# Kernel optimization log

Hardware: AMD Instinct MI355X
Metric: run time of the kernel (lower is better)

The kernel has to match this reference:

```python
import jax, jax.numpy as jnp
import numpy as np
import math

B, H, W = 4, 256, 256
S = 256          # num_superpixels
ZD = 128         # z_dim
GC = 256         # g_channels
NBLK = 8


def setup_inputs() -> dict:
    key = jax.random.key(0)
    ks = jax.random.split(key, 12)
    rn = lambda k, shp, s=1.0: jax.random.normal(k, shp, jnp.float32) * s
    return {
        "z": rn(ks[0], (B, ZD)),
        "images": rn(ks[1], (B, 3, H, W)),
        "segments": jax.random.randint(ks[2], (B, H, W), 0, S).astype(jnp.int32),
        # row-stochastic-ish adjacency scale keeps 8 propagations stable
        "A": rn(ks[3], (B, S, S), 1.0 / math.sqrt(S)),
        # WSConv2d weights: init N(0,1); forward multiplies input by sqrt(2/(in*k*k))
        "proj_w": rn(ks[4], (GC, 3 + ZD)), "proj_b": jnp.zeros((GC,), jnp.float32),
        "blk_proj_w": rn(ks[5], (NBLK, GC, GC)), "blk_proj_b": jnp.zeros((NBLK, GC), jnp.float32),
        "ada1_w": rn(ks[6], (NBLK, 2 * GC, GC)), "ada1_b": jnp.zeros((NBLK, 2 * GC), jnp.float32),
        "ada2_w": rn(ks[7], (NBLK, 2 * GC, 2 * GC)), "ada2_b": jnp.zeros((NBLK, 2 * GC), jnp.float32),
        # plain Conv2d 3x3 layers in upsample head
        "up1_w": rn(ks[8], (GC // 2, GC, 3, 3), 0.02), "up1_b": jnp.zeros((GC // 2,), jnp.float32),
        "up2_w": rn(ks[9], (3, GC // 2, 3, 3), 0.02), "up2_b": jnp.zeros((3,), jnp.float32),
    }


def _ws1x1(x, w, b):
    # WSConv2d with 1x1 kernel over node dim: x [B,Cin,S] -> [B,Cout,S]
    scale = math.sqrt(2.0 / w.shape[1])
    return jnp.einsum('oc,bcs->bos', w, x) * scale + b[None, :, None]


def _conv3(x, w, b):
    y = jax.lax.conv_general_dilated(x, w, (1, 1), 'SAME',
                                     dimension_numbers=('NCHW', 'OIHW', 'NCHW'))
    return y + b[None, :, None, None]


def _forward(z, images, A, proj_w, proj_b, blk_proj_w, blk_proj_b,
             ada1_w, ada1_b, ada2_w, ada2_b, up1_w, up1_b, up2_w, up2_b,
             segments):
    Bn, _, Hn, Wn = images.shape
    N = Hn * Wn
    flat = images.reshape(Bn, 3, N)            # [B,3,N]
    seg = segments.reshape(Bn, N)              # [B,N] int

    # superpixel mean pooling (math of one_hot^T @ flat / counts, as segment-sum)
    seg_sum = jax.vmap(lambda f, s: jax.ops.segment_sum(f, s, num_segments=S))(
        flat.transpose(0, 2, 1), seg)          # [B,S,3]
    counts = jax.vmap(lambda s: jax.ops.segment_sum(
        jnp.ones(s.shape, jnp.float32), s, num_segments=S))(seg)  # [B,S]
    feats = seg_sum / (counts[..., None] + 1e-6)

    z_rep = jnp.broadcast_to(z[:, None, :], (Bn, S, ZD))
    x = jnp.concatenate([feats, z_rep], axis=2).transpose(0, 2, 1)  # [B,3+ZD,S]
    x = _ws1x1(x, proj_w, proj_b)                                   # [B,GC,S]

    for i in range(NBLK):
        h = _ws1x1(x, blk_proj_w[i], blk_proj_b[i])
        # A @ feat : out[b,c,i] = sum_j A[b,i,j] h[b,c,j]
        h = jnp.einsum('bij,bcj->bci', A, h)
        # AdaIN: style from global mean over nodes
        m = h.mean(axis=2, keepdims=True)                    # [B,GC,1]
        s1 = jax.nn.leaky_relu(_ws1x1(m, ada1_w[i], ada1_b[i]), 0.2)
        style = _ws1x1(s1, ada2_w[i], ada2_b[i])             # [B,2GC,1]
        gamma, beta = jnp.split(style, 2, axis=1)
        h = gamma * h + beta
        x = jax.nn.leaky_relu(h, 0.2)                        # dropout=0 (eval)

    # broadcast superpixel feats back to pixels (math of one_hot @ sup_feats)
    sup_feats = x.transpose(0, 2, 1)                         # [B,S,GC]
    pix = jnp.take_along_axis(sup_feats, seg[:, :, None].astype(jnp.int32), axis=1)  # [B,N,GC]
    pix = pix.transpose(0, 2, 1).reshape(Bn, GC, Hn, Wn)

    y = jax.nn.leaky_relu(_conv3(pix, up1_w, up1_b), 0.2)
    y = _conv3(y, up2_w, up2_b)                              # [B,3,H,W]
    # InstanceNorm2d(3), affine=False, eps=1e-5
    mu = y.mean((2, 3), keepdims=True)
    var = y.var((2, 3), keepdims=True)
    y = (y - mu) / jnp.sqrt(var + 1e-5)
    return jnp.tanh(y)


def reference(z, images, segments, A, proj_w, proj_b, blk_proj_w, blk_proj_b,
              ada1_w, ada1_b, ada2_w, ada2_b, up1_w, up1_b, up2_w, up2_b):
    return _forward(z, images, A, proj_w, proj_b, blk_proj_w, blk_proj_b,
                    ada1_w, ada1_b, ada2_w, ada2_b, up1_w, up1_b, up2_w, up2_b,
                    segments)
```

## Files before the change

### kernel.cpp

```cpp
#include <hip/hip_runtime.h>
#include <cmath>

#define BB 4
#define SS 256
#define ZDIM 128
#define GCH 256
#define NBLKS 8
#define NPIX 65536
#define U1C 128

__device__ __forceinline__ float lrelu(float x){ return x >= 0.f ? x : 0.2f*x; }

__global__ void k_pool(const float* __restrict__ img, const int* __restrict__ seg,
                       float* __restrict__ segsum, float* __restrict__ counts){
  __shared__ float ls[SS*4];
  int t = threadIdx.x;
  for(int j=t;j<SS*4;j+=256) ls[j]=0.f;
  __syncthreads();
  int b = blockIdx.x >> 6;
  int base = blockIdx.x*1024;
  for(int it=0; it<4; it++){
    int idx = base + it*256 + t;
    int n = idx & (NPIX-1);
    int s = seg[idx];
    atomicAdd(&ls[s*4+0], img[(b*3+0)*NPIX+n]);
    atomicAdd(&ls[s*4+1], img[(b*3+1)*NPIX+n]);
    atomicAdd(&ls[s*4+2], img[(b*3+2)*NPIX+n]);
    atomicAdd(&ls[s*4+3], 1.0f);
  }
  __syncthreads();
  for(int j=t;j<SS*4;j+=256){
    int s = j>>2, c = j&3;
    float vv = ls[j];
    if(vv != 0.f){
      if(c<3) atomicAdd(&segsum[(b*SS+s)*3+c], vv);
      else    atomicAdd(&counts[b*SS+s], vv);
    }
  }
}

__global__ __launch_bounds__(256) void k_prepA(const float* __restrict__ A,
                                               float* __restrict__ At){
  __shared__ float t[32][33];
  int b = blockIdx.z;
  int bx = blockIdx.x*32, by = blockIdx.y*32;
  int lx = threadIdx.x & 31, ly4 = (threadIdx.x >> 5)*4;
  #pragma unroll
  for(int r=0;r<4;r++)
    t[ly4+r][lx] = A[(b<<16) + ((by+ly4+r)<<8) + bx + lx];
  __syncthreads();
  #pragma unroll
  for(int r=0;r<4;r++)
    At[(b<<16) + ((bx+ly4+r)<<8) + by + lx] = t[lx][ly4+r];
}

__global__ void k_prepW(const float* __restrict__ w1, const float* __restrict__ w2,
                        float* __restrict__ wT, float* __restrict__ w2t){
  int idx = blockIdx.x*256 + threadIdx.x;
  if(idx < 294912){
    int o = idx & 127; int r = idx >> 7; int c = r & 255; int k = r >> 8;
    wT[idx] = w1[(o*GCH + c)*9 + k];
  } else if(idx < 294912 + 3456){
    int t = idx - 294912;
    int cc = t & 7;
    int oc = (t >> 3) % 3;
    int sg = (t / 24) & 3;
    int g  = (t / 96) & 3;
    int k  = t / 384;
    w2t[t] = w2[oc*1152 + (g*32 + sg*8 + cc)*9 + k];
  }
}

__global__ void k_x0(const float* __restrict__ segsum, const float* __restrict__ counts,
                     const float* __restrict__ z, const float* __restrict__ pw,
                     const float* __restrict__ pb, float sc, float* __restrict__ xp){
  int i = blockIdx.x*64 + (threadIdx.x & 63);
  int o = blockIdx.y*4  + (threadIdx.x >> 6);
  int b = blockIdx.z;
  float cnt = counts[b*SS+i] + 1e-6f;
  float f0 = segsum[(b*SS+i)*3+0]/cnt;
  float f1 = segsum[(b*SS+i)*3+1]/cnt;
  float f2 = segsum[(b*SS+i)*3+2]/cnt;
  const float* wr = pw + o*131;
  float acc = wr[0]*f0 + wr[1]*f1 + wr[2]*f2;
  const float* zb = z + b*ZDIM;
  #pragma unroll 8
  for(int j=0;j<ZDIM;j++) acc += wr[3+j]*zb[j];
  xp[(b*GCH+o)*SS + i] = acc*sc + pb[o];
}

__global__ __launch_bounds__(512) void k_gemm(const float* __restrict__ xp,
        const float* __restrict__ bw, const float* __restrict__ bb,
        const float* __restrict__ At, float sc,
        float* __restrict__ h2, float* __restrict__ m){
  int c0 = blockIdx.x*4;
  int b  = blockIdx.y;
  int j  = threadIdx.x & 255;
  int half = threadIdx.x >> 8;
  __shared__ float wl[4][256];
  __shared__ float h1l[4][260];
  __shared__ float red[4][4];
  wl[half*2+0][j] = bw[(c0+half*2+0)*GCH + j];
  wl[half*2+1][j] = bw[(c0+half*2+1)*GCH + j];
  __syncthreads();
  const float* xb = xp + b*GCH*SS + j;
  float a0 = 0.f, a1 = 0.f;
  int ch = half*2;
  #pragma unroll 8
  for(int k=0;k<GCH;k++){
    float xv = xb[k*SS];
    a0 += wl[ch][k]*xv;
    a1 += wl[ch+1][k]*xv;
  }
  h1l[ch][j]   = a0*sc + bb[c0+ch];
  h1l[ch+1][j] = a1*sc + bb[c0+ch+1];
  __syncthreads();
  const float* ab = At + b*SS*SS + j;
  float r0 = 0.f, r1 = 0.f;
  #pragma unroll 2
  for(int jj=0;jj<SS;jj+=4){
    float4 h0 = *(const float4*)&h1l[ch][jj];
    float4 h1v = *(const float4*)&h1l[ch+1][jj];
    float av0 = ab[jj*SS], av1 = ab[(jj+1)*SS], av2 = ab[(jj+2)*SS], av3 = ab[(jj+3)*SS];
    r0 += h0.x*av0 + h0.y*av1 + h0.z*av2 + h0.w*av3;
    r1 += h1v.x*av0 + h1v.y*av1 + h1v.z*av2 + h1v.w*av3;
  }
  h2[(b*GCH+c0+ch)*SS + j]   = r0;
  h2[(b*GCH+c0+ch+1)*SS + j] = r1;
  float s0 = r0, s1v = r1;
  for(int off=32; off; off>>=1){ s0 += __shfl_down(s0,off); s1v += __shfl_down(s1v,off); }
  int w3 = (threadIdx.x >> 6) & 3;
  if((j&63)==0){ red[ch][w3] = s0; red[ch+1][w3] = s1v; }
  __syncthreads();
  if(threadIdx.x < 4)
    m[b*GCH + c0 + threadIdx.x] =
      (red[threadIdx.x][0]+red[threadIdx.x][1]+red[threadIdx.x][2]+red[threadIdx.x][3])*(1.f/256.f);
}

__global__ __launch_bounds__(512) void k_s12(const float* __restrict__ m,
        const float* __restrict__ a1w, const float* __restrict__ a1b,
        const float* __restrict__ a2w, const float* __restrict__ a2b,
        const float* __restrict__ h2, float sc1, float sc2, float* __restrict__ xp){
  int q = blockIdx.x;
  int tid = threadIdx.x;
  int lane = tid & 63, wv = tid >> 6;
  int grp = lane >> 3, ll = lane & 7;
  __shared__ float4 ml4[256];
  __shared__ float s1l[4][512];
  __shared__ float gbl[4][16];
  if(tid < 256) ml4[tid] = ((const float4*)m)[tid];
  __syncthreads();
  #pragma unroll 2
  for(int pass=0; pass<8; pass++){
    int row = wv*64 + pass*8 + grp;
    const float4* ar = (const float4*)(a1w + row*GCH) + ll;
    float p0=0.f,p1=0.f,p2=0.f,p3=0.f;
    #pragma unroll
    for(int j=0;j<8;j++){
      float4 w4 = ar[j*8];
      float4 m0 = ml4[0*64 + j*8 + ll];
      float4 m1 = ml4[1*64 + j*8 + ll];
      float4 m2 = ml4[2*64 + j*8 + ll];
      float4 m3 = ml4[3*64 + j*8 + ll];
      p0 += w4.x*m0.x + w4.y*m0.y + w4.z*m0.z + w4.w*m0.w;
      p1 += w4.x*m1.x + w4.y*m1.y + w4.z*m1.z + w4.w*m1.w;
      p2 += w4.x*m2.x + w4.y*m2.y + w4.z*m2.z + w4.w*m2.w;
      p3 += w4.x*m3.x + w4.y*m3.y + w4.z*m3.z + w4.w*m3.w;
    }
    #pragma unroll
    for(int off=1; off<8; off<<=1){
      p0 += __shfl_xor(p0,off); p1 += __shfl_xor(p1,off);
      p2 += __shfl_xor(p2,off); p3 += __shfl_xor(p3,off);
    }
    if(ll == 0){
      float bv = a1b[row];
      int sidx = ((row & 7) << 6) + (row >> 3);
      s1l[0][sidx] = lrelu(p0*sc1 + bv);
      s1l[1][sidx] = lrelu(p1*sc1 + bv);
      s1l[2][sidx] = lrelu(p2*sc1 + bv);
      s1l[3][sidx] = lrelu(p3*sc1 + bv);
    }
  }
  __syncthreads();
  float sA[4][8];
  #pragma unroll
  for(int b=0;b<4;b++)
    #pragma unroll
    for(int j=0;j<8;j++) sA[b][j] = s1l[b][j*64 + lane];
  #pragma unroll
  for(int r=0;r<2;r++){
    int ridx = wv*2 + r;
    int cc = ridx & 7;
    int t = (ridx < 8) ? (q*8 + cc) : (256 + q*8 + cc);
    const float* wr = a2w + t*512 + lane*8;
    float4 wa = *(const float4*)wr;
    float4 wb4 = *(const float4*)(wr+4);
    float p0 = wa.x*sA[0][0]+wa.y*sA[0][1]+wa.z*sA[0][2]+wa.w*sA[0][3]
             + wb4.x*sA[0][4]+wb4.y*sA[0][5]+wb4.z*sA[0][6]+wb4.w*sA[0][7];
    float p1 = wa.x*sA[1][0]+wa.y*sA[1][1]+wa.z*sA[1][2]+wa.w*sA[1][3]
             + wb4.x*sA[1][4]+wb4.y*sA[1][5]+wb4.z*sA[1][6]+wb4.w*sA[1][7];
    float p2 = wa.x*sA[2][0]+wa.y*sA[2][1]+wa.z*sA[2][2]+wa.w*sA[2][3]
             + wb4.x*sA[2][4]+wb4.y*sA[2][5]+wb4.z*sA[2][6]+wb4.w*sA[2][7];
    float p3 = wa.x*sA[3][0]+wa.y*sA[3][1]+wa.z*sA[3][2]+wa.w*sA[3][3]
             + wb4.x*sA[3][4]+wb4.y*sA[3][5]+wb4.z*sA[3][6]+wb4.w*sA[3][7];
    for(int off=32; off; off>>=1){
      p0 += __shfl_xor(p0,off); p1 += __shfl_xor(p1,off);
      p2 += __shfl_xor(p2,off); p3 += __shfl_xor(p3,off);
    }
    if(lane < 4){
      float p = lane==0 ? p0 : lane==1 ? p1 : lane==2 ? p2 : p3;
      gbl[lane][ridx] = p*sc2 + a2b[t];
    }
  }
  __syncthreads();
  int c0 = q*8;
  int jn = tid & 255;
  int hf = tid >> 8;
  #pragma unroll
  for(int b=0;b<4;b++){
    #pragma unroll
    for(int c2=0;c2<4;c2++){
      int cc = hf*4 + c2;
      float ga = gbl[b][cc], be = gbl[b][8+cc];
      float hv = h2[(b*GCH + c0+cc)*SS + jn];
      xp[(b*GCH + c0+cc)*SS + jn] = lrelu(ga*hv + be);
    }
  }
}

__global__ __launch_bounds__(256) void k_v(const float* __restrict__ xf,
        const float4* __restrict__ wT4, float4* __restrict__ v4){
  int s0 = blockIdx.x*16;
  int k  = blockIdx.y;
  int b  = blockIdx.z;
  int tid = threadIdx.x;
  __shared__ float4 wl[64][33];
  __shared__ float xft[256][16];
  for(int t = tid; t < 1024; t += 256){
    int c = t>>2, sf = t&3;
    *(float4*)&xft[c][sf*4] = *(const float4*)(xf + (b*GCH+c)*SS + s0 + sf*4);
  }
  int og = tid & 31, sh = tid >> 5;
  const float4* wb = wT4 + (size_t)k*GCH*32;
  float4 a0 = {0.f,0.f,0.f,0.f}, a1 = {0.f,0.f,0.f,0.f};
  for(int ct=0; ct<4; ct++){
    __syncthreads();
    for(int t = tid; t < 2048; t += 256){
      int cc = t>>5, o = t&31;
      wl[cc][o] = wb[(ct*64+cc)*32 + o];
    }
    __syncthreads();
    #pragma unroll 4
    for(int cc=0;cc<64;cc++){
      float4 w = wl[cc][og];
      int c = ct*64+cc;
      float x0v = xft[c][sh];
      float x1v = xft[c][8+sh];
      a0.x += w.x*x0v; a0.y += w.y*x0v; a0.z += w.z*x0v; a0.w += w.w*x0v;
      a1.x += w.x*x1v; a1.y += w.y*x1v; a1.z += w.z*x1v; a1.w += w.w*x1v;
    }
  }
  size_t base = (size_t)(b*9+k)*SS + s0;
  v4[(base + sh)*32 + og]     = a0;
  v4[(base + 8 + sh)*32 + og] = a1;
}

__global__ __launch_bounds__(256) void k_conv(const float4* __restrict__ v4,
        const int* __restrict__ seg, const float4* __restrict__ b14,
        const float* __restrict__ w2t, float* __restrict__ y2){
  __shared__ float4 y1t4[100*9];
  __shared__ int   segl[144];
  __shared__ float part[768];
  int bid = blockIdx.x;
  int x = bid & 7;
  int b = x >> 1;
  int sub = ((bid >> 3) << 1) + (x & 1);
  int g = sub & 3;
  int tile = sub >> 2;
  int x0p = (tile & 31)*8, y0p = (tile >> 5)*8;
  int tid = threadIdx.x;
  if(tid < 144){
    int r = tid/12, cc = tid%12;
    int gy = y0p - 2 + r, gx = x0p - 2 + cc;
    segl[tid] = (gy>=0 && gy<256 && gx>=0 && gx<256) ? seg[(b*256+gy)*256+gx] : -1;
  }
  __syncthreads();
  int o4 = tid & 7;
  const float4* vb = v4 + (size_t)(b*9)*SS*32 + g*8 + o4;
  float4 bias = b14[g*8 + o4];
  bool interior = (x0p >= 8 && x0p <= 240 && y0p >= 8 && y0p <= 240);
  if(interior){
    for(int task = tid; task < 800; task += 256){
      int pp = task >> 3;
      int py = pp/10, px = pp - py*10;
      float4 acc = bias;
      #pragma unroll
      for(int k=0;k<9;k++){
        int sidx = segl[(py + k/3)*12 + (px + k%3)];
        float4 vv = vb[(k*SS + sidx)*32];
        acc.x += vv.x; acc.y += vv.y; acc.z += vv.z; acc.w += vv.w;
      }
      float4 val;
      val.x = lrelu(acc.x); val.y = lrelu(acc.y);
      val.z = lrelu(acc.z); val.w = lrelu(acc.w);
      y1t4[pp*9 + o4] = val;
    }
  } else {
    for(int task = tid; task < 800; task += 256){
      int pp = task >> 3;
      int py = pp/10, px = pp - py*10;
      int gy = y0p - 1 + py, gx = x0p - 1 + px;
      bool pix_ok = (gy>=0 && gy<256 && gx>=0 && gx<256);
      float4 acc = bias;
      #pragma unroll
      for(int k=0;k<9;k++){
        int sidx = segl[(py + k/3)*12 + (px + k%3)];
        int sidx0 = sidx < 0 ? 0 : sidx;
        float msk = sidx < 0 ? 0.f : 1.f;
        float4 vv = vb[(k*SS + sidx0)*32];
        acc.x += msk*vv.x; acc.y += msk*vv.y; acc.z += msk*vv.z; acc.w += msk*vv.w;
      }
      float4 val;
      val.x = pix_ok ? lrelu(acc.x) : 0.f;
      val.y = pix_ok ? lrelu(acc.y) : 0.f;
      val.z = pix_ok ? lrelu(acc.z) : 0.f;
      val.w = pix_ok ? lrelu(acc.w) : 0.f;
      y1t4[pp*9 + o4] = val;
    }
  }
  __syncthreads();
  int pxo = tid & 63, sg = tid >> 6;
  int sgu = __builtin_amdgcn_readfirstlane(sg);
  const float* wk0 = w2t + (g*4 + sgu)*24;
  int ty = pxo >> 3, tx = pxo & 7;
  float p0=0.f,p1=0.f,p2=0.f;
  #pragma unroll
  for(int k=0;k<9;k++){
    int pp0 = (ty + k/3)*10 + (tx + k%3);
    float4 ya = y1t4[pp0*9 + sgu*2];
    float4 yb = y1t4[pp0*9 + sgu*2 + 1];
    const float* wk = wk0 + k*384;
    p0 += wk[0]*ya.x + wk[1]*ya.y + wk[2]*ya.z + wk[3]*ya.w
        + wk[4]*yb.x + wk[5]*yb.y + wk[6]*yb.z + wk[7]*yb.w;
    p1 += wk[8]*ya.x + wk[9]*ya.y + wk[10]*ya.z + wk[11]*ya.w
        + wk[12]*yb.x + wk[13]*yb.y + wk[14]*yb.z + wk[15]*yb.w;
    p2 += wk[16]*ya.x + wk[17]*ya.y + wk[18]*ya.z + wk[19]*ya.w
        + wk[20]*yb.x + wk[21]*yb.y + wk[22]*yb.z + wk[23]*yb.w;
  }
  part[tid]     = p0;
  part[256+tid] = p1;
  part[512+tid] = p2;
  __syncthreads();
  if(tid < 64){
    float s0 = part[tid]    +part[tid+64]    +part[tid+128]    +part[tid+192];
    float s1 = part[256+tid]+part[256+tid+64]+part[256+tid+128]+part[256+tid+192];
    float s2 = part[512+tid]+part[512+tid+64]+part[512+tid+128]+part[512+tid+192];
    int gy = y0p + (tid>>3), gx = x0p + (tid&7);
    int nidx = gy*256+gx;
    atomicAdd(&y2[(b*3+0)*NPIX+nidx], s0);
    atomicAdd(&y2[(b*3+1)*NPIX+nidx], s1);
    atomicAdd(&y2[(b*3+2)*NPIX+nidx], s2);
  }
}

__global__ void k_stats(const float* __restrict__ y2, double* __restrict__ stats){
  int bc = blockIdx.x;
  int chunk = blockIdx.y;
  const float* p = y2 + (size_t)bc*NPIX + chunk*8192;
  int t = threadIdx.x;
  double s=0.0, q=0.0;
  for(int i=t;i<8192;i+=256){ double vv = (double)p[i]; s+=vv; q+=vv*vv; }
  __shared__ double rs[256], rq[256];
  rs[t]=s; rq[t]=q; __syncthreads();
  for(int st=128; st; st>>=1){ if(t<st){rs[t]+=rs[t+st]; rq[t]+=rq[t+st];} __syncthreads(); }
  if(t==0){ atomicAdd(&stats[bc*2], rs[0]); atomicAdd(&stats[bc*2+1], rq[0]); }
}

__global__ void k_norm(const float* __restrict__ y2, const double* __restrict__ stats,
                       float* __restrict__ out){
  int idx = blockIdx.x*256+threadIdx.x;
  int bu = idx >> 16;
  double mu  = stats[bu*2+0] * (1.0/65536.0);
  double ex2 = stats[bu*2+1] * (1.0/65536.0);
  double var = ex2 - mu*mu;
  float inv = (float)(1.0/sqrt(var + 1e-5));
  float mf = (float)mu;
  out[idx] = tanhf((y2[idx]-mf)*inv);
}

extern "C" void kernel_launch(void* const* d_in, const int* in_sizes, int n_in,
                              void* d_out, int out_size, void* d_ws, size_t ws_size,
                              hipStream_t stream) {
  const float* z   = (const float*)d_in[0];
  const float* img = (const float*)d_in[1];
  const int*   seg = (const int*)d_in[2];
  const float* A   = (const float*)d_in[3];
  const float* pw  = (const float*)d_in[4];
  const float* pb  = (const float*)d_in[5];
  const float* bw  = (const float*)d_in[6];
  const float* bb  = (const float*)d_in[7];
  const float* a1w = (const float*)d_in[8];
  const float* a1b = (const float*)d_in[9];
  const float* a2w = (const float*)d_in[10];
  const float* a2b = (const float*)d_in[11];
  const float* w1  = (const float*)d_in[12];
  const float* b1  = (const float*)d_in[13];
  const float* w2  = (const float*)d_in[14];
  const float* b2  = (const float*)d_in[15]; (void)b2;
  float* out = (float*)d_out;

  float* ws = (float*)d_ws;
  float* segsum = ws;
  float* counts = ws + 3072;
  float* m      = ws + 4096;
  double* stats = (double*)(ws + 5120);
  float* xp  = ws + 5248;
  float* h2  = xp + 262144;
  float* At  = h2 + 262144;
  float* wT  = At + 262144;
  float* v   = wT + 294912;
  float* y2  = v + 1179648;
  float* w2t = y2 + 786432;

  hipMemsetAsync(ws, 0, 5248*sizeof(float), stream);
  hipMemsetAsync(y2, 0, 786432*sizeof(float), stream);

  float sProj = (float)sqrt(2.0/131.0);
  float s256  = (float)sqrt(2.0/256.0);
  float s512  = (float)sqrt(2.0/512.0);

  k_pool <<<256, 256, 0, stream>>>(img, seg, segsum, counts);
  k_prepA<<<dim3(8,8,4), 256, 0, stream>>>(A, At);
  k_prepW<<<1166, 256, 0, stream>>>(w1, w2, wT, w2t);
  k_x0   <<<dim3(4,64,4), 256, 0, stream>>>(segsum, counts, z, pw, pb, sProj, xp);

  for(int blk=0; blk<NBLKS; blk++){
    k_gemm<<<dim3(64,4), 512, 0, stream>>>(xp, bw + blk*GCH*GCH, bb + blk*GCH,
                                           At, s256, h2, m);
    k_s12 <<<32, 512, 0, stream>>>(m, a1w + blk*512*GCH, a1b + blk*512,
                                   a2w + blk*512*512, a2b + blk*512,
                                   h2, s256, s512, xp);
  }

  k_v   <<<dim3(16,9,4), 256, 0, stream>>>(xp, (const float4*)wT, (float4*)v);
  k_conv<<<16384, 256, 0, stream>>>((const float4*)v, seg, (const float4*)b1, w2t, y2);
  k_stats<<<dim3(12,8), 256, 0, stream>>>(y2, stats);
  k_norm<<<3072, 256, 0, stream>>>(y2, stats, out);
}
```

Before: 408.7 us.

## Fuse pooling, projection and graph blocks into persistent kernel with grid barriers

```diff
diff --git a/kernel.cpp b/kernel.cpp
--- a/kernel.cpp
+++ b/kernel.cpp
@@ -11,220 +11,203 @@
 
 __device__ __forceinline__ float lrelu(float x){ return x >= 0.f ? x : 0.2f*x; }
 
-__global__ void k_pool(const float* __restrict__ img, const int* __restrict__ seg,
-                       float* __restrict__ segsum, float* __restrict__ counts){
-  __shared__ float ls[SS*4];
-  int t = threadIdx.x;
-  for(int j=t;j<SS*4;j+=256) ls[j]=0.f;
+__device__ __forceinline__ void gridbar(int* bar, int target){
   __syncthreads();
-  int b = blockIdx.x >> 6;
-  int base = blockIdx.x*1024;
-  for(int it=0; it<4; it++){
-    int idx = base + it*256 + t;
-    int n = idx & (NPIX-1);
-    int s = seg[idx];
-    atomicAdd(&ls[s*4+0], img[(b*3+0)*NPIX+n]);
-    atomicAdd(&ls[s*4+1], img[(b*3+1)*NPIX+n]);
-    atomicAdd(&ls[s*4+2], img[(b*3+2)*NPIX+n]);
-    atomicAdd(&ls[s*4+3], 1.0f);
+  if(threadIdx.x == 0){
+    __hip_atomic_fetch_add(bar, 1, __ATOMIC_RELEASE, __HIP_MEMORY_SCOPE_AGENT);
+    while(__hip_atomic_load(bar, __ATOMIC_ACQUIRE, __HIP_MEMORY_SCOPE_AGENT) < target)
+      __builtin_amdgcn_s_sleep(2);
   }
   __syncthreads();
-  for(int j=t;j<SS*4;j+=256){
-    int s = j>>2, c = j&3;
-    float vv = ls[j];
-    if(vv != 0.f){
-      if(c<3) atomicAdd(&segsum[(b*SS+s)*3+c], vv);
-      else    atomicAdd(&counts[b*SS+s], vv);
-    }
-  }
-}
-
-__global__ __launch_bounds__(256) void k_prepA(const float* __restrict__ A,
-                                               float* __restrict__ At){
-  __shared__ float t[32][33];
-  int b = blockIdx.z;
-  int bx = blockIdx.x*32, by = blockIdx.y*32;
-  int lx = threadIdx.x & 31, ly4 = (threadIdx.x >> 5)*4;
-  #pragma unroll
-  for(int r=0;r<4;r++)
-    t[ly4+r][lx] = A[(b<<16) + ((by+ly4+r)<<8) + bx + lx];
-  __syncthreads();
-  #pragma unroll
-  for(int r=0;r<4;r++)
-    At[(b<<16) + ((bx+ly4+r)<<8) + by + lx] = t[lx][ly4+r];
-}
-
-__global__ void k_prepW(const float* __restrict__ w1, const float* __restrict__ w2,
-                        float* __restrict__ wT, float* __restrict__ w2t){
-  int idx = blockIdx.x*256 + threadIdx.x;
-  if(idx < 294912){
-    int o = idx & 127; int r = idx >> 7; int c = r & 255; int k = r >> 8;
-    wT[idx] = w1[(o*GCH + c)*9 + k];
-  } else if(idx < 294912 + 3456){
-    int t = idx - 294912;
-    int cc = t & 7;
-    int oc = (t >> 3) % 3;
-    int sg = (t / 24) & 3;
-    int g  = (t / 96) & 3;
-    int k  = t / 384;
-    w2t[t] = w2[oc*1152 + (g*32 + sg*8 + cc)*9 + k];
-  }
-}
-
-__global__ void k_x0(const float* __restrict__ segsum, const float* __restrict__ counts,
-                     const float* __restrict__ z, const float* __restrict__ pw,
-                     const float* __restrict__ pb, float sc, float* __restrict__ xp){
-  int i = blockIdx.x*64 + (threadIdx.x & 63);
-  int o = blockIdx.y*4  + (threadIdx.x >> 6);
-  int b = blockIdx.z;
-  float cnt = counts[b*SS+i] + 1e-6f;
-  float f0 = segsum[(b*SS+i)*3+0]/cnt;
-  float f1 = segsum[(b*SS+i)*3+1]/cnt;
-  float f2 = segsum[(b*SS+i)*3+2]/cnt;
-  const float* wr = pw + o*131;
-  float acc = wr[0]*f0 + wr[1]*f1 + wr[2]*f2;
-  const float* zb = z + b*ZDIM;
-  #pragma unroll 8
-  for(int j=0;j<ZDIM;j++) acc += wr[3+j]*zb[j];
-  xp[(b*GCH+o)*SS + i] = acc*sc + pb[o];
-}
-
-__global__ __launch_bounds__(512) void k_gemm(const float* __restrict__ xp,
-        const float* __restrict__ bw, const float* __restrict__ bb,
-        const float* __restrict__ At, float sc,
-        float* __restrict__ h2, float* __restrict__ m){
-  int c0 = blockIdx.x*4;
-  int b  = blockIdx.y;
-  int j  = threadIdx.x & 255;
-  int half = threadIdx.x >> 8;
+}
+
+__global__ __launch_bounds__(256) void k_prep(const float* __restrict__ A,
+        const float* __restrict__ w1, const float* __restrict__ w2,
+        float* __restrict__ At, float* __restrict__ wT, float* __restrict__ w2t){
+  int bid = blockIdx.x;
+  if(bid < 256){
+    __shared__ float t[32][33];
+    int b = bid >> 6;
+    int bx = (bid & 7)*32, by = ((bid >> 3) & 7)*32;
+    int lx = threadIdx.x & 31, ly4 = (threadIdx.x >> 5)*4;
+    #pragma unroll
+    for(int r=0;r<4;r++)
+      t[ly4+r][lx] = A[(b<<16) + ((by+ly4+r)<<8) + bx + lx];
+    __syncthreads();
+    #pragma unroll
+    for(int r=0;r<4;r++)
+      At[(b<<16) + ((bx+ly4+r)<<8) + by + lx] = t[lx][ly4+r];
+  } else {
+    int idx = (bid-256)*256 + threadIdx.x;
+    if(idx < 294912){
+      int o = idx & 127; int r = idx >> 7; int c = r & 255; int k = r >> 8;
+      wT[idx] = w1[(o*GCH + c)*9 + k];
+    } else if(idx < 294912 + 3456){
+      int t2 = idx - 294912;
+      int cc = t2 & 7;
+      int oc = (t2 >> 3) % 3;
+      int sg = (t2 / 24) & 3;
+      int g  = (t2 / 96) & 3;
+      int k  = t2 / 384;
+      w2t[t2] = w2[oc*1152 + (g*32 + sg*8 + cc)*9 + k];
+    }
+  }
+}
+
+__global__ __launch_bounds__(512) void k_mega(
+    const float* __restrict__ img, const int* __restrict__ seg,
+    float* __restrict__ segsum, float* __restrict__ counts,
+    const float* __restrict__ z, const float* __restrict__ pw,
+    const float* __restrict__ pb, const float* __restrict__ At,
+    const float* __restrict__ bw_all, const float* __restrict__ bb_all,
+    const float* __restrict__ a1w_all, const float* __restrict__ a1b_all,
+    const float* __restrict__ a2w_all, const float* __restrict__ a2b_all,
+    float* __restrict__ xp, float* __restrict__ h2,
+    float* __restrict__ m, float* __restrict__ s1g, int* __restrict__ bar,
+    float sProj, float sc1, float sc2){
+  int bid = blockIdx.x;
+  int tid = threadIdx.x;
+  int lane = tid & 63, wv = tid >> 6;
+  __shared__ float ls[1024];
   __shared__ float wl[4][256];
   __shared__ float h1l[4][260];
   __shared__ float red[4][4];
-  wl[half*2+0][j] = bw[(c0+half*2+0)*GCH + j];
-  wl[half*2+1][j] = bw[(c0+half*2+1)*GCH + j];
-  __syncthreads();
-  const float* xb = xp + b*GCH*SS + j;
-  float a0 = 0.f, a1 = 0.f;
-  int ch = half*2;
-  #pragma unroll 8
-  for(int k=0;k<GCH;k++){
-    float xv = xb[k*SS];
-    a0 += wl[ch][k]*xv;
-    a1 += wl[ch+1][k]*xv;
-  }
-  h1l[ch][j]   = a0*sc + bb[c0+ch];
-  h1l[ch+1][j] = a1*sc + bb[c0+ch+1];
-  __syncthreads();
-  const float* ab = At + b*SS*SS + j;
-  float r0 = 0.f, r1 = 0.f;
-  #pragma unroll 2
-  for(int jj=0;jj<SS;jj+=4){
-    float4 h0 = *(const float4*)&h1l[ch][jj];
-    float4 h1v = *(const float4*)&h1l[ch+1][jj];
-    float av0 = ab[jj*SS], av1 = ab[(jj+1)*SS], av2 = ab[(jj+2)*SS], av3 = ab[(jj+3)*SS];
-    r0 += h0.x*av0 + h0.y*av1 + h0.z*av2 + h0.w*av3;
-    r1 += h1v.x*av0 + h1v.y*av1 + h1v.z*av2 + h1v.w*av3;
-  }
-  h2[(b*GCH+c0+ch)*SS + j]   = r0;
-  h2[(b*GCH+c0+ch+1)*SS + j] = r1;
-  float s0 = r0, s1v = r1;
-  for(int off=32; off; off>>=1){ s0 += __shfl_down(s0,off); s1v += __shfl_down(s1v,off); }
-  int w3 = (threadIdx.x >> 6) & 3;
-  if((j&63)==0){ red[ch][w3] = s0; red[ch+1][w3] = s1v; }
-  __syncthreads();
-  if(threadIdx.x < 4)
-    m[b*GCH + c0 + threadIdx.x] =
-      (red[threadIdx.x][0]+red[threadIdx.x][1]+red[threadIdx.x][2]+red[threadIdx.x][3])*(1.f/256.f);
-}
-
-__global__ __launch_bounds__(512) void k_s12(const float* __restrict__ m,
-        const float* __restrict__ a1w, const float* __restrict__ a1b,
-        const float* __restrict__ a2w, const float* __restrict__ a2b,
-        const float* __restrict__ h2, float sc1, float sc2, float* __restrict__ xp){
-  int q = blockIdx.x;
-  int tid = threadIdx.x;
-  int lane = tid & 63, wv = tid >> 6;
-  int grp = lane >> 3, ll = lane & 7;
-  __shared__ float4 ml4[256];
-  __shared__ float s1l[4][512];
-  __shared__ float gbl[4][16];
-  if(tid < 256) ml4[tid] = ((const float4*)m)[tid];
-  __syncthreads();
-  #pragma unroll 2
-  for(int pass=0; pass<8; pass++){
-    int row = wv*64 + pass*8 + grp;
-    const float4* ar = (const float4*)(a1w + row*GCH) + ll;
-    float p0=0.f,p1=0.f,p2=0.f,p3=0.f;
+  __shared__ float gbl[8];
+  int bt = 0;
+
+  {
+    for(int j=tid;j<1024;j+=512) ls[j]=0.f;
+    __syncthreads();
+    int b = bid >> 6;
+    int base = bid*1024;
     #pragma unroll
-    for(int j=0;j<8;j++){
-      float4 w4 = ar[j*8];
-      float4 m0 = ml4[0*64 + j*8 + ll];
-      float4 m1 = ml4[1*64 + j*8 + ll];
-      float4 m2 = ml4[2*64 + j*8 + ll];
-      float4 m3 = ml4[3*64 + j*8 + ll];
-      p0 += w4.x*m0.x + w4.y*m0.y + w4.z*m0.z + w4.w*m0.w;
-      p1 += w4.x*m1.x + w4.y*m1.y + w4.z*m1.z + w4.w*m1.w;
-      p2 += w4.x*m2.x + w4.y*m2.y + w4.z*m2.z + w4.w*m2.w;
-      p3 += w4.x*m3.x + w4.y*m3.y + w4.z*m3.z + w4.w*m3.w;
-    }
+    for(int it2=0; it2<2; it2++){
+      int idx = base + it2*512 + tid;
+      int n = idx & (NPIX-1);
+      int s = seg[idx];
+      atomicAdd(&ls[s*4+0], img[(b*3+0)*NPIX+n]);
+      atomicAdd(&ls[s*4+1], img[(b*3+1)*NPIX+n]);
+      atomicAdd(&ls[s*4+2], img[(b*3+2)*NPIX+n]);
+      atomicAdd(&ls[s*4+3], 1.0f);
+    }
+    __syncthreads();
+    for(int j=tid;j<1024;j+=512){
+      int s = j>>2, c = j&3;
+      float vv = ls[j];
+      if(vv != 0.f){
+        if(c<3) atomicAdd(&segsum[(b*SS+s)*3+c], vv);
+        else    atomicAdd(&counts[b*SS+s], vv);
+      }
+    }
+  }
+  bt += 256; gridbar(bar, bt);
+
+  {
+    int b = bid & 3, og = bid >> 2;
+    int i = tid & 255;
+    int oo = tid >> 8;
+    float cnt = counts[b*SS+i] + 1e-6f;
+    float f0 = segsum[(b*SS+i)*3+0]/cnt;
+    float f1 = segsum[(b*SS+i)*3+1]/cnt;
+    float f2 = segsum[(b*SS+i)*3+2]/cnt;
+    const float* zb = z + b*ZDIM;
     #pragma unroll
-    for(int off=1; off<8; off<<=1){
-      p0 += __shfl_xor(p0,off); p1 += __shfl_xor(p1,off);
-      p2 += __shfl_xor(p2,off); p3 += __shfl_xor(p3,off);
-    }
-    if(ll == 0){
-      float bv = a1b[row];
-      int sidx = ((row & 7) << 6) + (row >> 3);
-      s1l[0][sidx] = lrelu(p0*sc1 + bv);
-      s1l[1][sidx] = lrelu(p1*sc1 + bv);
-      s1l[2][sidx] = lrelu(p2*sc1 + bv);
-      s1l[3][sidx] = lrelu(p3*sc1 + bv);
-    }
-  }
-  __syncthreads();
-  float sA[4][8];
-  #pragma unroll
-  for(int b=0;b<4;b++)
-    #pragma unroll
-    for(int j=0;j<8;j++) sA[b][j] = s1l[b][j*64 + lane];
-  #pragma unroll
-  for(int r=0;r<2;r++){
-    int ridx = wv*2 + r;
-    int cc = ridx & 7;
-    int t = (ridx < 8) ? (q*8 + cc) : (256 + q*8 + cc);
-    const float* wr = a2w + t*512 + lane*8;
-    float4 wa = *(const float4*)wr;
-    float4 wb4 = *(const float4*)(wr+4);
-    float p0 = wa.x*sA[0][0]+wa.y*sA[0][1]+wa.z*sA[0][2]+wa.w*sA[0][3]
-             + wb4.x*sA[0][4]+wb4.y*sA[0][5]+wb4.z*sA[0][6]+wb4.w*sA[0][7];
-    float p1 = wa.x*sA[1][0]+wa.y*sA[1][1]+wa.z*sA[1][2]+wa.w*sA[1][3]
-             + wb4.x*sA[1][4]+wb4.y*sA[1][5]+wb4.z*sA[1][6]+wb4.w*sA[1][7];
-    float p2 = wa.x*sA[2][0]+wa.y*sA[2][1]+wa.z*sA[2][2]+wa.w*sA[2][3]
-             + wb4.x*sA[2][4]+wb4.y*sA[2][5]+wb4.z*sA[2][6]+wb4.w*sA[2][7];
-    float p3 = wa.x*sA[3][0]+wa.y*sA[3][1]+wa.z*sA[3][2]+wa.w*sA[3][3]
-             + wb4.x*sA[3][4]+wb4.y*sA[3][5]+wb4.z*sA[3][6]+wb4.w*sA[3][7];
-    for(int off=32; off; off>>=1){
-      p0 += __shfl_xor(p0,off); p1 += __shfl_xor(p1,off);
-      p2 += __shfl_xor(p2,off); p3 += __shfl_xor(p3,off);
-    }
-    if(lane < 4){
-      float p = lane==0 ? p0 : lane==1 ? p1 : lane==2 ? p2 : p3;
-      gbl[lane][ridx] = p*sc2 + a2b[t];
-    }
-  }
-  __syncthreads();
-  int c0 = q*8;
-  int jn = tid & 255;
-  int hf = tid >> 8;
-  #pragma unroll
-  for(int b=0;b<4;b++){
-    #pragma unroll
-    for(int c2=0;c2<4;c2++){
-      int cc = hf*4 + c2;
-      float ga = gbl[b][cc], be = gbl[b][8+cc];
-      float hv = h2[(b*GCH + c0+cc)*SS + jn];
-      xp[(b*GCH + c0+cc)*SS + jn] = lrelu(ga*hv + be);
-    }
+    for(int o2=0;o2<2;o2++){
+      int o = og*4 + oo*2 + o2;
+      const float* wr = pw + o*131;
+      float acc = wr[0]*f0 + wr[1]*f1 + wr[2]*f2;
+      #pragma unroll 8
+      for(int j=0;j<ZDIM;j++) acc += wr[3+j]*zb[j];
+      xp[(b*GCH+o)*SS + i] = acc*sProj + pb[o];
+    }
+  }
+  bt += 256; gridbar(bar, bt);
+
+  for(int it=0; it<NBLKS; it++){
+    const float* bw  = bw_all  + it*GCH*GCH;
+    const float* bb  = bb_all  + it*GCH;
+    const float* a1w = a1w_all + it*512*GCH;
+    const float* a1b = a1b_all + it*512;
+    const float* a2w = a2w_all + it*512*512;
+    const float* a2b = a2b_all + it*512;
+
+    {
+      int c0 = (bid >> 2)*4;
+      int b  = bid & 3;
+      int j  = tid & 255;
+      int half = tid >> 8;
+      wl[half*2+0][j] = bw[(c0+half*2+0)*GCH + j];
+      wl[half*2+1][j] = bw[(c0+half*2+1)*GCH + j];
+      __syncthreads();
+      const float* xb = xp + b*GCH*SS + j;
+      float a0 = 0.f, a1 = 0.f;
+      int ch = half*2;
+      #pragma unroll 8
+      for(int k=0;k<GCH;k++){
+        float xv = xb[k*SS];
+        a0 += wl[ch][k]*xv;
+        a1 += wl[ch+1][k]*xv;
+      }
+      h1l[ch][j]   = a0*sc1 + bb[c0+ch];
+      h1l[ch+1][j] = a1*sc1 + bb[c0+ch+1];
+      __syncthreads();
+      const float* ab = At + b*SS*SS + j;
+      float r0 = 0.f, r1 = 0.f;
+      #pragma unroll 2
+      for(int jj=0;jj<SS;jj+=4){
+        float4 h0 = *(const float4*)&h1l[ch][jj];
+        float4 h1v = *(const float4*)&h1l[ch+1][jj];
+        float av0 = ab[jj*SS], av1 = ab[(jj+1)*SS], av2 = ab[(jj+2)*SS], av3 = ab[(jj+3)*SS];
+        r0 += h0.x*av0 + h0.y*av1 + h0.z*av2 + h0.w*av3;
+        r1 += h1v.x*av0 + h1v.y*av1 + h1v.z*av2 + h1v.w*av3;
+      }
+      h2[(b*GCH+c0+ch)*SS + j]   = r0;
+      h2[(b*GCH+c0+ch+1)*SS + j] = r1;
+      float s0 = r0, s1v = r1;
+      for(int off=32; off; off>>=1){ s0 += __shfl_down(s0,off); s1v += __shfl_down(s1v,off); }
+      int w3 = (tid >> 6) & 3;
+      if((j&63)==0){ red[ch][w3] = s0; red[ch+1][w3] = s1v; }
+      __syncthreads();
+      if(tid < 4)
+        m[b*GCH + c0 + tid] =
+          (red[tid][0]+red[tid][1]+red[tid][2]+red[tid][3])*(1.f/256.f);
+    }
+    bt += 256; gridbar(bar, bt);
+
+    {
+      int r = bid*2 + (wv >> 2);
+      int b = wv & 3;
+      float4 w4 = ((const float4*)(a1w + r*GCH))[lane];
+      float4 m4 = ((const float4*)(m + b*GCH))[lane];
+      float p = w4.x*m4.x + w4.y*m4.y + w4.z*m4.z + w4.w*m4.w;
+      for(int off=32; off; off>>=1) p += __shfl_xor(p, off);
+      if(lane == 0) s1g[b*512 + r] = lrelu(p*sc1 + a1b[r]);
+    }
+    bt += 256; gridbar(bar, bt);
+
+    {
+      int c = bid;
+      int b = wv & 3;
+      int part = wv >> 2;
+      int t = part*256 + c;
+      const float4* wr = (const float4*)(a2w + t*512) + lane*2;
+      const float4* sr = (const float4*)(s1g + b*512) + lane*2;
+      float4 wa = wr[0], wb4 = wr[1], sa = sr[0], sb = sr[1];
+      float p = wa.x*sa.x + wa.y*sa.y + wa.z*sa.z + wa.w*sa.w
+              + wb4.x*sb.x + wb4.y*sb.y + wb4.z*sb.z + wb4.w*sb.w;
+      for(int off=32; off; off>>=1) p += __shfl_xor(p, off);
+      if(lane == 0) gbl[part*4 + b] = p*sc2 + a2b[t];
+      __syncthreads();
+      int b2 = tid >> 7;
+      int j2 = (tid & 127)*2;
+      float ga = gbl[b2], be = gbl[4 + b2];
+      float2 hv = *(const float2*)&h2[(b2*GCH + c)*SS + j2];
+      float2 xv;
+      xv.x = lrelu(ga*hv.x + be);
+      xv.y = lrelu(ga*hv.y + be);
+      *(float2*)&xp[(b2*GCH + c)*SS + j2] = xv;
+    }
+    bt += 256; gridbar(bar, bt);
   }
 }
 
@@ -378,13 +361,13 @@
 
 __global__ void k_norm(const float* __restrict__ y2, const double* __restrict__ stats,
                        float* __restrict__ out){
-  int idx = blockIdx.x*256+threadIdx.x;
-  int bu = idx >> 16;
+  int bu = (blockIdx.x*256) >> 16;
   double mu  = stats[bu*2+0] * (1.0/65536.0);
   double ex2 = stats[bu*2+1] * (1.0/65536.0);
   double var = ex2 - mu*mu;
   float inv = (float)(1.0/sqrt(var + 1e-5));
   float mf = (float)mu;
+  int idx = blockIdx.x*256+threadIdx.x;
   out[idx] = tanhf((y2[idx]-mf)*inv);
 }
 
@@ -413,8 +396,10 @@
   float* segsum = ws;
   float* counts = ws + 3072;
   float* m      = ws + 4096;
-  double* stats = (double*)(ws + 5120);
-  float* xp  = ws + 5248;
+  float* s1g    = ws + 5120;
+  double* stats = (double*)(ws + 7168);
+  int*   bar    = (int*)(ws + 7216);
+  float* xp  = ws + 7296;
   float* h2  = xp + 262144;
   float* At  = h2 + 262144;
   float* wT  = At + 262144;
@@ -422,26 +407,17 @@
   float* y2  = v + 1179648;
   float* w2t = y2 + 786432;
 
-  hipMemsetAsync(ws, 0, 5248*sizeof(float), stream);
+  hipMemsetAsync(ws, 0, 7296*sizeof(float), stream);
   hipMemsetAsync(y2, 0, 786432*sizeof(float), stream);
 
   float sProj = (float)sqrt(2.0/131.0);
   float s256  = (float)sqrt(2.0/256.0);
   float s512  = (float)sqrt(2.0/512.0);
 
-  k_pool <<<256, 256, 0, stream>>>(img, seg, segsum, counts);
-  k_prepA<<<dim3(8,8,4), 256, 0, stream>>>(A, At);
-  k_prepW<<<1166, 256, 0, stream>>>(w1, w2, wT, w2t);
-  k_x0   <<<dim3(4,64,4), 256, 0, stream>>>(segsum, counts, z, pw, pb, sProj, xp);
-
-  for(int blk=0; blk<NBLKS; blk++){
-    k_gemm<<<dim3(64,4), 512, 0, stream>>>(xp, bw + blk*GCH*GCH, bb + blk*GCH,
-                                           At, s256, h2, m);
-    k_s12 <<<32, 512, 0, stream>>>(m, a1w + blk*512*GCH, a1b + blk*512,
-                                   a2w + blk*512*512, a2b + blk*512,
-                                   h2, s256, s512, xp);
-  }
-
+  k_prep<<<256 + 1166, 256, 0, stream>>>(A, w1, w2, At, wT, w2t);
+  k_mega<<<256, 512, 0, stream>>>(img, seg, segsum, counts, z, pw, pb, At,
+                                  bw, bb, a1w, a1b, a2w, a2b,
+                                  xp, h2, m, s1g, bar, sProj, s256, s512);
   k_v   <<<dim3(16,9,4), 256, 0, stream>>>(xp, (const float4*)wT, (float4*)v);
   k_conv<<<16384, 256, 0, stream>>>((const float4*)v, seg, (const float4*)b1, w2t, y2);
   k_stats<<<dim3(12,8), 256, 0, stream>>>(y2, stats);
```

New measurement: 639.0 us. 1.56x slower.

## Interleave node features and adjacency in float4 channel groups for vectorized GEMM loads

Applied to the files above, without the earlier changes.

```diff
diff --git a/kernel.cpp b/kernel.cpp
--- a/kernel.cpp
+++ b/kernel.cpp
@@ -39,108 +39,127 @@
   }
 }
 
-__global__ __launch_bounds__(256) void k_prepA(const float* __restrict__ A,
-                                               float* __restrict__ At){
-  __shared__ float t[32][33];
-  int b = blockIdx.z;
-  int bx = blockIdx.x*32, by = blockIdx.y*32;
-  int lx = threadIdx.x & 31, ly4 = (threadIdx.x >> 5)*4;
-  #pragma unroll
-  for(int r=0;r<4;r++)
-    t[ly4+r][lx] = A[(b<<16) + ((by+ly4+r)<<8) + bx + lx];
-  __syncthreads();
-  #pragma unroll
-  for(int r=0;r<4;r++)
-    At[(b<<16) + ((bx+ly4+r)<<8) + by + lx] = t[lx][ly4+r];
-}
-
-__global__ void k_prepW(const float* __restrict__ w1, const float* __restrict__ w2,
-                        float* __restrict__ wT, float* __restrict__ w2t){
-  int idx = blockIdx.x*256 + threadIdx.x;
-  if(idx < 294912){
-    int o = idx & 127; int r = idx >> 7; int c = r & 255; int k = r >> 8;
-    wT[idx] = w1[(o*GCH + c)*9 + k];
-  } else if(idx < 294912 + 3456){
-    int t = idx - 294912;
-    int cc = t & 7;
-    int oc = (t >> 3) % 3;
-    int sg = (t / 24) & 3;
-    int g  = (t / 96) & 3;
-    int k  = t / 384;
-    w2t[t] = w2[oc*1152 + (g*32 + sg*8 + cc)*9 + k];
-  }
-}
-
-__global__ void k_x0(const float* __restrict__ segsum, const float* __restrict__ counts,
-                     const float* __restrict__ z, const float* __restrict__ pw,
-                     const float* __restrict__ pb, float sc, float* __restrict__ xp){
-  int i = blockIdx.x*64 + (threadIdx.x & 63);
-  int o = blockIdx.y*4  + (threadIdx.x >> 6);
-  int b = blockIdx.z;
+__global__ __launch_bounds__(256) void k_prep(const float* __restrict__ A,
+        const float* __restrict__ w1, const float* __restrict__ w2,
+        float* __restrict__ At2, float* __restrict__ wT, float* __restrict__ w2t){
+  int bid = blockIdx.x;
+  if(bid < 256){
+    __shared__ float t[32][33];
+    int b = bid >> 6;
+    int bx = (bid & 7)*32, by = ((bid >> 3) & 7)*32;
+    int lx = threadIdx.x & 31, ly4 = (threadIdx.x >> 5)*4;
+    #pragma unroll
+    for(int r=0;r<4;r++)
+      t[ly4+r][lx] = A[(b<<16) + ((by+ly4+r)<<8) + bx + lx];
+    __syncthreads();
+    #pragma unroll
+    for(int r=0;r<4;r++){
+      int jj = bx + ly4 + r;
+      int i  = by + lx;
+      At2[(b<<16) + ((jj>>2)<<10) + (i<<2) + (jj&3)] = t[lx][ly4+r];
+    }
+  } else {
+    int idx = (bid-256)*256 + threadIdx.x;
+    if(idx < 294912){
+      int o = idx & 127; int r = idx >> 7; int c = r & 255; int k = r >> 8;
+      wT[idx] = w1[(o*GCH + c)*9 + k];
+    } else if(idx < 294912 + 3456){
+      int t2 = idx - 294912;
+      int cc = t2 & 7;
+      int oc = (t2 >> 3) % 3;
+      int sg = (t2 / 24) & 3;
+      int g  = (t2 / 96) & 3;
+      int k  = t2 / 384;
+      w2t[t2] = w2[oc*1152 + (g*32 + sg*8 + cc)*9 + k];
+    }
+  }
+}
+
+__global__ __launch_bounds__(256) void k_x0(const float* __restrict__ segsum,
+        const float* __restrict__ counts, const float* __restrict__ z,
+        const float* __restrict__ pw, const float* __restrict__ pb,
+        float sc, float4* __restrict__ xp2){
+  int og = blockIdx.x;
+  int b  = blockIdx.y;
+  int i  = threadIdx.x;
   float cnt = counts[b*SS+i] + 1e-6f;
   float f0 = segsum[(b*SS+i)*3+0]/cnt;
   float f1 = segsum[(b*SS+i)*3+1]/cnt;
   float f2 = segsum[(b*SS+i)*3+2]/cnt;
-  const float* wr = pw + o*131;
-  float acc = wr[0]*f0 + wr[1]*f1 + wr[2]*f2;
   const float* zb = z + b*ZDIM;
-  #pragma unroll 8
-  for(int j=0;j<ZDIM;j++) acc += wr[3+j]*zb[j];
-  xp[(b*GCH+o)*SS + i] = acc*sc + pb[o];
-}
-
-__global__ __launch_bounds__(512) void k_gemm(const float* __restrict__ xp,
+  float vals[4];
+  #pragma unroll
+  for(int oo=0;oo<4;oo++){
+    int o = og*4 + oo;
+    const float* wr = pw + o*131;
+    float acc = wr[0]*f0 + wr[1]*f1 + wr[2]*f2;
+    #pragma unroll 8
+    for(int j=0;j<ZDIM;j++) acc += wr[3+j]*zb[j];
+    vals[oo] = acc*sc + pb[o];
+  }
+  float4 o4 = {vals[0], vals[1], vals[2], vals[3]};
+  xp2[(b*64+og)*256 + i] = o4;
+}
+
+__global__ __launch_bounds__(512) void k_gemm(const float4* __restrict__ xp2,
         const float* __restrict__ bw, const float* __restrict__ bb,
-        const float* __restrict__ At, float sc,
+        const float4* __restrict__ At2, float sc,
         float* __restrict__ h2, float* __restrict__ m){
   int c0 = blockIdx.x*4;
   int b  = blockIdx.y;
-  int j  = threadIdx.x & 255;
-  int half = threadIdx.x >> 8;
-  __shared__ float wl[4][256];
-  __shared__ float h1l[4][260];
+  int tid = threadIdx.x;
+  int j  = tid & 255;
+  int half = tid >> 8;
+  int ch0 = c0 + half*2;
+  __shared__ float4 wl4[4][64];
+  __shared__ float4 h1l4[4][66];
   __shared__ float red[4][4];
-  wl[half*2+0][j] = bw[(c0+half*2+0)*GCH + j];
-  wl[half*2+1][j] = bw[(c0+half*2+1)*GCH + j];
-  __syncthreads();
-  const float* xb = xp + b*GCH*SS + j;
+  for(int t = tid; t < 1024; t += 512){
+    int row = t >> 8, jj = t & 255;
+    ((float*)&wl4[row][0])[jj] = bw[(c0+row)*GCH + jj];
+  }
+  __syncthreads();
+  const float4* xb = xp2 + (b*64)*256 + j;
   float a0 = 0.f, a1 = 0.f;
-  int ch = half*2;
+  int r0i = half*2, r1i = half*2+1;
   #pragma unroll 8
-  for(int k=0;k<GCH;k++){
-    float xv = xb[k*SS];
-    a0 += wl[ch][k]*xv;
-    a1 += wl[ch+1][k]*xv;
-  }
-  h1l[ch][j]   = a0*sc + bb[c0+ch];
-  h1l[ch+1][j] = a1*sc + bb[c0+ch+1];
-  __syncthreads();
-  const float* ab = At + b*SS*SS + j;
+  for(int kg=0;kg<64;kg++){
+    float4 x = xb[kg*256];
+    float4 w0 = wl4[r0i][kg];
+    float4 w1 = wl4[r1i][kg];
+    a0 += w0.x*x.x + w0.y*x.y + w0.z*x.z + w0.w*x.w;
+    a1 += w1.x*x.x + w1.y*x.y + w1.z*x.z + w1.w*x.w;
+  }
+  ((float*)&h1l4[r0i][0])[j] = a0*sc + bb[ch0];
+  ((float*)&h1l4[r1i][0])[j] = a1*sc + bb[ch0+1];
+  __syncthreads();
+  const float4* ab = At2 + (b*64)*256 + j;
   float r0 = 0.f, r1 = 0.f;
-  #pragma unroll 2
-  for(int jj=0;jj<SS;jj+=4){
-    float4 h0 = *(const float4*)&h1l[ch][jj];
-    float4 h1v = *(const float4*)&h1l[ch+1][jj];
-    float av0 = ab[jj*SS], av1 = ab[(jj+1)*SS], av2 = ab[(jj+2)*SS], av3 = ab[(jj+3)*SS];
-    r0 += h0.x*av0 + h0.y*av1 + h0.z*av2 + h0.w*av3;
-    r1 += h1v.x*av0 + h1v.y*av1 + h1v.z*av2 + h1v.w*av3;
-  }
-  h2[(b*GCH+c0+ch)*SS + j]   = r0;
-  h2[(b*GCH+c0+ch+1)*SS + j] = r1;
+  #pragma unroll 8
+  for(int kg=0;kg<64;kg++){
+    float4 a = ab[kg*256];
+    float4 h0 = h1l4[r0i][kg];
+    float4 h1 = h1l4[r1i][kg];
+    r0 += a.x*h0.x + a.y*h0.y + a.z*h0.z + a.w*h0.w;
+    r1 += a.x*h1.x + a.y*h1.y + a.z*h1.z + a.w*h1.w;
+  }
+  h2[(b*GCH+ch0)*SS + j]   = r0;
+  h2[(b*GCH+ch0+1)*SS + j] = r1;
   float s0 = r0, s1v = r1;
   for(int off=32; off; off>>=1){ s0 += __shfl_down(s0,off); s1v += __shfl_down(s1v,off); }
-  int w3 = (threadIdx.x >> 6) & 3;
-  if((j&63)==0){ red[ch][w3] = s0; red[ch+1][w3] = s1v; }
-  __syncthreads();
-  if(threadIdx.x < 4)
-    m[b*GCH + c0 + threadIdx.x] =
-      (red[threadIdx.x][0]+red[threadIdx.x][1]+red[threadIdx.x][2]+red[threadIdx.x][3])*(1.f/256.f);
+  int w3 = (tid >> 6) & 3;
+  if((j&63)==0){ red[r0i][w3] = s0; red[r1i][w3] = s1v; }
+  __syncthreads();
+  if(tid < 4)
+    m[b*GCH + c0 + tid] =
+      (red[tid][0]+red[tid][1]+red[tid][2]+red[tid][3])*(1.f/256.f);
 }
 
 __global__ __launch_bounds__(512) void k_s12(const float* __restrict__ m,
         const float* __restrict__ a1w, const float* __restrict__ a1b,
         const float* __restrict__ a2w, const float* __restrict__ a2b,
-        const float* __restrict__ h2, float sc1, float sc2, float* __restrict__ xp){
+        const float* __restrict__ h2, float sc1, float sc2,
+        float4* __restrict__ xp2){
   int q = blockIdx.x;
   int tid = threadIdx.x;
   int lane = tid & 63, wv = tid >> 6;
@@ -213,32 +232,36 @@
     }
   }
   __syncthreads();
-  int c0 = q*8;
-  int jn = tid & 255;
-  int hf = tid >> 8;
+  int j = tid & 255;
+  int cg2 = tid >> 8;
+  int cbase = q*8 + cg2*4;
+  int cg = cbase >> 2;
   #pragma unroll
   for(int b=0;b<4;b++){
-    #pragma unroll
-    for(int c2=0;c2<4;c2++){
-      int cc = hf*4 + c2;
-      float ga = gbl[b][cc], be = gbl[b][8+cc];
-      float hv = h2[(b*GCH + c0+cc)*SS + jn];
-      xp[(b*GCH + c0+cc)*SS + jn] = lrelu(ga*hv + be);
-    }
-  }
-}
-
-__global__ __launch_bounds__(256) void k_v(const float* __restrict__ xf,
+    float4 o;
+    o.x = lrelu(gbl[b][cg2*4+0]*h2[(b*GCH + cbase+0)*SS + j] + gbl[b][8+cg2*4+0]);
+    o.y = lrelu(gbl[b][cg2*4+1]*h2[(b*GCH + cbase+1)*SS + j] + gbl[b][8+cg2*4+1]);
+    o.z = lrelu(gbl[b][cg2*4+2]*h2[(b*GCH + cbase+2)*SS + j] + gbl[b][8+cg2*4+2]);
+    o.w = lrelu(gbl[b][cg2*4+3]*h2[(b*GCH + cbase+3)*SS + j] + gbl[b][8+cg2*4+3]);
+    xp2[(b*64 + cg)*256 + j] = o;
+  }
+}
+
+__global__ __launch_bounds__(256) void k_v(const float4* __restrict__ xp2,
         const float4* __restrict__ wT4, float4* __restrict__ v4){
   int s0 = blockIdx.x*16;
   int k  = blockIdx.y;
   int b  = blockIdx.z;
   int tid = threadIdx.x;
   __shared__ float4 wl[64][33];
-  __shared__ float xft[256][16];
+  __shared__ float xft[256][17];
   for(int t = tid; t < 1024; t += 256){
-    int c = t>>2, sf = t&3;
-    *(float4*)&xft[c][sf*4] = *(const float4*)(xf + (b*GCH+c)*SS + s0 + sf*4);
+    int cg = t >> 4, si = t & 15;
+    float4 xv = xp2[(b*64 + cg)*256 + s0 + si];
+    xft[cg*4+0][si] = xv.x;
+    xft[cg*4+1][si] = xv.y;
+    xft[cg*4+2][si] = xv.z;
+    xft[cg*4+3][si] = xv.w;
   }
   int og = tid & 31, sh = tid >> 5;
   const float4* wb = wT4 + (size_t)k*GCH*32;
@@ -378,13 +401,13 @@
 
 __global__ void k_norm(const float* __restrict__ y2, const double* __restrict__ stats,
                        float* __restrict__ out){
-  int idx = blockIdx.x*256+threadIdx.x;
-  int bu = idx >> 16;
+  int bu = (blockIdx.x*256) >> 16;
   double mu  = stats[bu*2+0] * (1.0/65536.0);
   double ex2 = stats[bu*2+1] * (1.0/65536.0);
   double var = ex2 - mu*mu;
   float inv = (float)(1.0/sqrt(var + 1e-5));
   float mf = (float)mu;
+  int idx = blockIdx.x*256+threadIdx.x;
   out[idx] = tanhf((y2[idx]-mf)*inv);
 }
 
@@ -414,10 +437,10 @@
   float* counts = ws + 3072;
   float* m      = ws + 4096;
   double* stats = (double*)(ws + 5120);
-  float* xp  = ws + 5248;
-  float* h2  = xp + 262144;
-  float* At  = h2 + 262144;
-  float* wT  = At + 262144;
+  float* xp2 = ws + 5248;
+  float* h2  = xp2 + 262144;
+  float* At2 = h2 + 262144;
+  float* wT  = At2 + 262144;
   float* v   = wT + 294912;
   float* y2  = v + 1179648;
   float* w2t = y2 + 786432;
@@ -429,20 +452,22 @@
   float s256  = (float)sqrt(2.0/256.0);
   float s512  = (float)sqrt(2.0/512.0);
 
-  k_pool <<<256, 256, 0, stream>>>(img, seg, segsum, counts);
-  k_prepA<<<dim3(8,8,4), 256, 0, stream>>>(A, At);
-  k_prepW<<<1166, 256, 0, stream>>>(w1, w2, wT, w2t);
-  k_x0   <<<dim3(4,64,4), 256, 0, stream>>>(segsum, counts, z, pw, pb, sProj, xp);
+  k_pool<<<256, 256, 0, stream>>>(img, seg, segsum, counts);
+  k_prep<<<256 + 1166, 256, 0, stream>>>(A, w1, w2, At2, wT, w2t);
+  k_x0  <<<dim3(64,4), 256, 0, stream>>>(segsum, counts, z, pw, pb, sProj,
+                                         (float4*)xp2);
 
   for(int blk=0; blk<NBLKS; blk++){
-    k_gemm<<<dim3(64,4), 512, 0, stream>>>(xp, bw + blk*GCH*GCH, bb + blk*GCH,
-                                           At, s256, h2, m);
+    k_gemm<<<dim3(64,4), 512, 0, stream>>>((const float4*)xp2,
+                                           bw + blk*GCH*GCH, bb + blk*GCH,
+                                           (const float4*)At2, s256, h2, m);
     k_s12 <<<32, 512, 0, stream>>>(m, a1w + blk*512*GCH, a1b + blk*512,
                                    a2w + blk*512*512, a2b + blk*512,
-                                   h2, s256, s512, xp);
-  }
-
-  k_v   <<<dim3(16,9,4), 256, 0, stream>>>(xp, (const float4*)wT, (float4*)v);
+                                   h2, s256, s512, (float4*)xp2);
+  }
+
+  k_v   <<<dim3(16,9,4), 256, 0, stream>>>((const float4*)xp2, (const float4*)wT,
+                                           (float4*)v);
   k_conv<<<16384, 256, 0, stream>>>((const float4*)v, seg, (const float4*)b1, w2t, y2);
   k_stats<<<dim3(12,8), 256, 0, stream>>>(y2, stats);
   k_norm<<<3072, 256, 0, stream>>>(y2, stats, out);
```

Measured after the change: 372.9 us. -8.8%, faster.
